# Performance work log

Hardware: AMD Instinct MI355X
Metric: run time of the kernel (lower is better)

Reference implementation:

```python
import jax, jax.numpy as jnp
import numpy as np

N = 50000      # nodes
E = 800000     # edges
MUL = 32       # multiplicity of each irrep (32x0e + 32x1o)
SQRT3 = 3.0 ** 0.5


def setup_inputs() -> dict:
    key = jax.random.key(0)
    k = jax.random.split(key, 7)
    node_features = jax.random.normal(k[0], (N, 4 * MUL), dtype=jnp.float32)  # [N, 32 + 32*3]
    positions = jax.random.normal(k[1], (N, 3), dtype=jnp.float32)
    edge_src = jax.random.randint(k[2], (E,), 0, N, dtype=jnp.int32)
    edge_dst = jax.random.randint(k[3], (E,), 0, N, dtype=jnp.int32)
    tp_weight = jax.random.normal(k[4], (4 * MUL,), dtype=jnp.float32)  # tp.weight_numel = 128
    W_s = jax.random.normal(k[5], (2 * MUL, MUL), dtype=jnp.float32)    # linear: mid 0e (2 blocks) -> out 0e
    W_v = jax.random.normal(k[6], (2 * MUL, MUL), dtype=jnp.float32)    # linear: mid 1o (2 blocks) -> out 1o
    return dict(node_features=node_features, positions=positions,
                edge_src=edge_src, edge_dst=edge_dst,
                tp_weight=tp_weight, W_s=W_s, W_v=W_v)


def reference(node_features, positions, edge_src, edge_dst, tp_weight, W_s, W_v):
    # --- edge vectors and spherical harmonics (normalize=True, 'component') ---
    edge_vec = positions[edge_dst] - positions[edge_src]                       # [E,3]
    unit = edge_vec * jax.lax.rsqrt(jnp.sum(edge_vec * edge_vec, -1, keepdims=True) + 1e-12)
    sh1 = SQRT3 * unit                                                         # l=1 SH, component norm; sh0 == 1
    # --- gather source node features, split irreps ---
    src = node_features[edge_src]                                              # [E,128]
    s = src[:, :MUL]                                                           # [E,32]  scalars 32x0e
    v = src[:, MUL:].reshape(-1, MUL, 3)                                       # [E,32,3] vectors 32x1o
    w0, w1, w2, w3 = jnp.split(tp_weight, 4)                                   # per-path 'uvu' weights (u=32, v=1)
    # --- CG tensor product paths ---
    mid0 = w0 * s                                                              # 0e x 0e -> 0e
    mid1 = (w1 * s)[:, :, None] * sh1[:, None, :]                              # 0e x 1o -> 1o
    mid2 = w2[None, :, None] * v                                               # 1o x 0e -> 1o
    mid3 = w3 * (jnp.einsum('eum,em->eu', v, sh1) / SQRT3)                     # 1o x 1o -> 0e (w3j = delta/sqrt(3))
    messages = jnp.concatenate(
        [mid0, mid1.reshape(-1, 3 * MUL), mid2.reshape(-1, 3 * MUL), mid3], axis=-1)  # [E,256]
    # --- scatter-add messages to destination nodes ---
    agg = jax.ops.segment_sum(messages, edge_dst, num_segments=N)              # [N,256]
    a0 = agg[:, :MUL]
    a1 = agg[:, MUL:4 * MUL].reshape(N, MUL, 3)
    a2 = agg[:, 4 * MUL:7 * MUL].reshape(N, MUL, 3)
    a3 = agg[:, 7 * MUL:]
    # --- equivariant linear mix mid -> out (fan-in normalized per irrep) ---
    inv = np.float32(1.0 / np.sqrt(2 * MUL))
    out_s = (jnp.concatenate([a0, a3], axis=-1) @ W_s) * inv                   # [N,32]
    out_v = jnp.einsum('num,uo->nom', jnp.concatenate([a1, a2], axis=1), W_v) * inv  # [N,32,3]
    return jnp.concatenate([out_s, out_v.reshape(N, 3 * MUL)], axis=-1)        # [N,128]
```

## Files before the change

kernel.cpp:

```cpp
#include <hip/hip_runtime.h>
#include <hip/hip_fp16.h>

#define SQRT3 1.7320508075688772f
#define INV_SQRT3 0.5773502691896258f
#define CAP 64

#define WAVE_SYNC() do { asm volatile("s_waitcnt lgkmcnt(0)" ::: "memory"); \
                         __builtin_amdgcn_wave_barrier(); } while (0)

__global__ void prep_kernel(const float* __restrict__ feat, const float* __restrict__ pos,
                            const float* __restrict__ Ws, const float* __restrict__ Wv,
                            const float* __restrict__ tpw,
                            uint2* __restrict__ featH, float4* __restrict__ pos4,
                            int* __restrict__ cnt,
                            float* __restrict__ WS, float* __restrict__ WV, int N) {
    int i = blockIdx.x * blockDim.x + threadIdx.x;
    int totalF = N * 32;
    if (i < totalF) {
        int node = i >> 5, cl = i & 31;
        const float* fb = feat + (size_t)node * 128;
        float s  = fb[cl];
        float v0 = fb[32 + 3 * cl], v1 = fb[33 + 3 * cl], v2 = fb[34 + 3 * cl];
        __half2 h0 = __floats2half2_rn(s, v0);
        __half2 h1 = __floats2half2_rn(v1, v2);
        uint2 r;
        r.x = *(const unsigned int*)&h0;
        r.y = *(const unsigned int*)&h1;
        featH[i] = r;
        return;
    }
    int j = i - totalF;
    if (j < N) {
        pos4[j] = make_float4(pos[3 * j], pos[3 * j + 1], pos[3 * j + 2], 0.f);
        cnt[j] = 0;
        return;
    }
    int k = j - N;
    if (k < 2048) {
        int u = k >> 5;
        float ws = Ws[k], wv = Wv[k];
        if (u < 32) {
            WS[k] = 0.125f * tpw[u] * ws;
            WV[k] = 0.125f * tpw[32 + u] * wv;
        } else {
            int uu = u - 32;
            WS[k] = 0.125f * tpw[96 + uu] * INV_SQRT3 * ws;
            WV[k] = 0.125f * tpw[64 + uu] * wv;
        }
    }
}


__global__ void scatter_kernel(const int* __restrict__ esrc, const int* __restrict__ edst,
                               int* __restrict__ cnt, int* __restrict__ csrP, int E) {
    int t = blockIdx.x * blockDim.x + threadIdx.x;
    int e0 = t * 4;
    if (e0 + 4 <= E) {
        int4 s4 = *(const int4*)(esrc + e0);
        int4 d4 = *(const int4*)(edst + e0);
        int p;
        p = atomicAdd(&cnt[d4.x], 1); if (p < CAP) csrP[(size_t)d4.x * CAP + p] = s4.x;
        p = atomicAdd(&cnt[d4.y], 1); if (p < CAP) csrP[(size_t)d4.y * CAP + p] = s4.y;
        p = atomicAdd(&cnt[d4.z], 1); if (p < CAP) csrP[(size_t)d4.z * CAP + p] = s4.z;
        p = atomicAdd(&cnt[d4.w], 1); if (p < CAP) csrP[(size_t)d4.w * CAP + p] = s4.w;
    } else {
        for (int e = e0; e < E; ++e) {
            int d = edst[e];
            int p = atomicAdd(&cnt[d], 1);
            if (p < CAP) csrP[(size_t)d * CAP + p] = esrc[e];
        }
    }
}


__global__ __launch_bounds__(256) void node_kernel(
    const uint2* __restrict__ featH, const float4* __restrict__ pos4,
    const int* __restrict__ csrP, const int* __restrict__ cnt,
    const float* __restrict__ WS, const float* __restrict__ WV,
    float* __restrict__ out, int N)
{
    __shared__ float4 geom[4][64];
    __shared__ float  sS[4][68], sX[4][68], sY[4][68], sZ[4][68];
    int lane = threadIdx.x & 63;
    int w    = threadIdx.x >> 6;
    int node = blockIdx.x * 4 + w;
    if (node >= N) return;

    int deg = cnt[node];
    int len = deg < CAP ? deg : CAP;
    int half = lane >> 5;
    int cl   = lane & 31;

    float4 pd = pos4[node];

    if (lane < len) {
        int s = csrP[(size_t)node * CAP + lane];
        float4 ps = pos4[s];
        float ex = pd.x - ps.x, ey = pd.y - ps.y, ez = pd.z - ps.z;
        float rr = SQRT3 * rsqrtf(ex * ex + ey * ey + ez * ez + 1e-12f);
        geom[w][lane] = make_float4(rr * ex, rr * ey, rr * ez, __int_as_float(s));
    }
    WAVE_SYNC();

    float A0 = 0.f, A1x = 0.f, A1y = 0.f, A1z = 0.f;
    float V0 = 0.f, V1 = 0.f, V2 = 0.f, T3 = 0.f;

    int even = len & ~1;
    #pragma unroll 4
    for (int m = 0; m < even; m += 2) {
        float4 g = geom[w][m + half];
        int si = __float_as_int(g.w);
        uint2 fr = featH[(size_t)si * 32 + cl];
        float2 lo = __half22float2(*(const __half2*)&fr.x);
        float2 hi = __half22float2(*(const __half2*)&fr.y);
        A0 += lo.x;
        A1x = fmaf(lo.x, g.x, A1x); A1y = fmaf(lo.x, g.y, A1y); A1z = fmaf(lo.x, g.z, A1z);
        V0 += lo.y; V1 += hi.x; V2 += hi.y;
        T3 = fmaf(lo.y, g.x, fmaf(hi.x, g.y, fmaf(hi.y, g.z, T3)));
    }
    if (len & 1) {
        if (half == 0) {
            float4 g = geom[w][len - 1];
            int si = __float_as_int(g.w);
            uint2 fr = featH[(size_t)si * 32 + cl];
            float2 lo = __half22float2(*(const __half2*)&fr.x);
            float2 hi = __half22float2(*(const __half2*)&fr.y);
            A0 += lo.x;
            A1x = fmaf(lo.x, g.x, A1x); A1y = fmaf(lo.x, g.y, A1y); A1z = fmaf(lo.x, g.z, A1z);
            V0 += lo.y; V1 += hi.x; V2 += hi.y;
            T3 = fmaf(lo.y, g.x, fmaf(hi.x, g.y, fmaf(hi.y, g.z, T3)));
        }
    }

    A0 += __shfl_xor(A0, 32);  A1x += __shfl_xor(A1x, 32);
    A1y += __shfl_xor(A1y, 32); A1z += __shfl_xor(A1z, 32);
    V0 += __shfl_xor(V0, 32);  V1 += __shfl_xor(V1, 32);
    V2 += __shfl_xor(V2, 32);  T3 += __shfl_xor(T3, 32);

    int k = half ? (32 + cl) : cl;
    sS[w][k] = half ? T3 : A0;
    sX[w][k] = half ? V0 : A1x;
    sY[w][k] = half ? V1 : A1y;
    sZ[w][k] = half ? V2 : A1z;
    WAVE_SYNC();

    size_t ob = (size_t)node * 128;
    #pragma unroll
    for (int t = 0; t < 2; ++t) {
        int j = lane + 64 * t;
        const float *ap, *wp;
        if (j < 32) {
            ap = sS[w]; wp = WS + j;
        } else {
            int v = j - 32;
            int o = v / 3, mm = v - 3 * o;
            ap = (mm == 0) ? sX[w] : (mm == 1) ? sY[w] : sZ[w];
            wp = WV + o;
        }
        float r = 0.f;
        #pragma unroll
        for (int q = 0; q < 16; ++q) {
            float4 a = *(const float4*)(ap + 4 * q);
            r = fmaf(a.x, wp[(4 * q + 0) * 32], r);
            r = fmaf(a.y, wp[(4 * q + 1) * 32], r);
            r = fmaf(a.z, wp[(4 * q + 2) * 32], r);
            r = fmaf(a.w, wp[(4 * q + 3) * 32], r);
        }
        out[ob + j] = r;
    }
}

extern "C" void kernel_launch(void* const* d_in, const int* in_sizes, int n_in,
                              void* d_out, int out_size, void* d_ws, size_t ws_size,
                              hipStream_t stream) {
    const float* feat = (const float*)d_in[0];
    const float* pos  = (const float*)d_in[1];
    const int*   esrc = (const int*)d_in[2];
    const int*   edst = (const int*)d_in[3];
    const float* tpw  = (const float*)d_in[4];
    const float* Ws   = (const float*)d_in[5];
    const float* Wv   = (const float*)d_in[6];
    float* out = (float*)d_out;

    int N = in_sizes[0] / 128;
    int E = in_sizes[2];

    uint2*  featH = (uint2*)d_ws;
    float4* pos4  = (float4*)(featH + (size_t)N * 32);
    int*    csrP  = (int*)(pos4 + N);
    int*    cnt   = csrP + (size_t)N * CAP;
    float*  WS    = (float*)(cnt + N);
    float*  WV    = WS + 2048;

    const int tb = 256;
    int prepTot = N * 32 + N + 2048;
    int ebk = (E / 4 + tb) / tb;
    prep_kernel<<<(prepTot + tb - 1) / tb, tb, 0, stream>>>(feat, pos, Ws, Wv, tpw,
                                                            featH, pos4, cnt, WS, WV, N);
    scatter_kernel<<<ebk, tb, 0, stream>>>(esrc, edst, cnt, csrP, E);
    node_kernel<<<(N + 3) / 4, 256, 0, stream>>>(featH, pos4, csrP, cnt, WS, WV, out, N);
}
```

Measured before the change: 124.1 us.

## Fuse scatter and prep kernels, use 16-bit CSR indices and wider feature gathers

Merges the edge-scatter and feature/weight prep into one launch, zeroing counts with a memset instead of inside prep. CSR source indices are stored as 16-bit when N fits, which halves that buffer's traffic. Each lane now gathers a uint4 (two channels), so four edges are processed per step across quarter-waves, followed by a two-level shuffle reduction. The mixing weights are transposed so each output reads contiguous float4s. The extra accumulators raise register pressure, and the int fallback path for large N overlaps csrU storage, so the workspace layout changes.

```diff
diff --git a/kernel.cpp b/kernel.cpp
--- a/kernel.cpp
+++ b/kernel.cpp
@@ -8,13 +8,37 @@
 #define WAVE_SYNC() do { asm volatile("s_waitcnt lgkmcnt(0)" ::: "memory"); \
                          __builtin_amdgcn_wave_barrier(); } while (0)
 
-__global__ void prep_kernel(const float* __restrict__ feat, const float* __restrict__ pos,
-                            const float* __restrict__ Ws, const float* __restrict__ Wv,
-                            const float* __restrict__ tpw,
-                            uint2* __restrict__ featH, float4* __restrict__ pos4,
-                            int* __restrict__ cnt,
-                            float* __restrict__ WS, float* __restrict__ WV, int N) {
-    int i = blockIdx.x * blockDim.x + threadIdx.x;
+template<typename IDX>
+__global__ void build_kernel(const int* __restrict__ esrc, const int* __restrict__ edst,
+                             const float* __restrict__ feat, const float* __restrict__ pos,
+                             const float* __restrict__ Ws, const float* __restrict__ Wv,
+                             const float* __restrict__ tpw,
+                             int* __restrict__ cnt, IDX* __restrict__ csrP,
+                             uint2* __restrict__ featH, float4* __restrict__ pos4,
+                             float* __restrict__ WST, float* __restrict__ WVT,
+                             int N, int E, int sblocks) {
+    int b = blockIdx.x;
+    if (b < sblocks) {
+        int t = b * blockDim.x + threadIdx.x;
+        int e0 = t * 4;
+        if (e0 + 4 <= E) {
+            int4 s4 = *(const int4*)(esrc + e0);
+            int4 d4 = *(const int4*)(edst + e0);
+            int p;
+            p = atomicAdd(&cnt[d4.x], 1); if (p < CAP) csrP[(size_t)d4.x * CAP + p] = (IDX)s4.x;
+            p = atomicAdd(&cnt[d4.y], 1); if (p < CAP) csrP[(size_t)d4.y * CAP + p] = (IDX)s4.y;
+            p = atomicAdd(&cnt[d4.z], 1); if (p < CAP) csrP[(size_t)d4.z * CAP + p] = (IDX)s4.z;
+            p = atomicAdd(&cnt[d4.w], 1); if (p < CAP) csrP[(size_t)d4.w * CAP + p] = (IDX)s4.w;
+        } else {
+            for (int e = e0; e < E; ++e) {
+                int d = edst[e];
+                int p = atomicAdd(&cnt[d], 1);
+                if (p < CAP) csrP[(size_t)d * CAP + p] = (IDX)esrc[e];
+            }
+        }
+        return;
+    }
+    int i = (b - sblocks) * blockDim.x + threadIdx.x;
     int totalF = N * 32;
     if (i < totalF) {
         int node = i >> 5, cl = i & 31;
@@ -32,51 +56,32 @@
     int j = i - totalF;
     if (j < N) {
         pos4[j] = make_float4(pos[3 * j], pos[3 * j + 1], pos[3 * j + 2], 0.f);
-        cnt[j] = 0;
         return;
     }
     int k = j - N;
     if (k < 2048) {
-        int u = k >> 5;
+        int u = k >> 5, c = k & 31;
         float ws = Ws[k], wv = Wv[k];
+        float fs, fv;
         if (u < 32) {
-            WS[k] = 0.125f * tpw[u] * ws;
-            WV[k] = 0.125f * tpw[32 + u] * wv;
+            fs = 0.125f * tpw[u] * ws;
+            fv = 0.125f * tpw[32 + u] * wv;
         } else {
             int uu = u - 32;
-            WS[k] = 0.125f * tpw[96 + uu] * INV_SQRT3 * ws;
-            WV[k] = 0.125f * tpw[64 + uu] * wv;
-        }
+            fs = 0.125f * tpw[96 + uu] * INV_SQRT3 * ws;
+            fv = 0.125f * tpw[64 + uu] * wv;
+        }
+        WST[c * 64 + u] = fs;
+        WVT[c * 64 + u] = fv;
     }
 }
 
 
-__global__ void scatter_kernel(const int* __restrict__ esrc, const int* __restrict__ edst,
-                               int* __restrict__ cnt, int* __restrict__ csrP, int E) {
-    int t = blockIdx.x * blockDim.x + threadIdx.x;
-    int e0 = t * 4;
-    if (e0 + 4 <= E) {
-        int4 s4 = *(const int4*)(esrc + e0);
-        int4 d4 = *(const int4*)(edst + e0);
-        int p;
-        p = atomicAdd(&cnt[d4.x], 1); if (p < CAP) csrP[(size_t)d4.x * CAP + p] = s4.x;
-        p = atomicAdd(&cnt[d4.y], 1); if (p < CAP) csrP[(size_t)d4.y * CAP + p] = s4.y;
-        p = atomicAdd(&cnt[d4.z], 1); if (p < CAP) csrP[(size_t)d4.z * CAP + p] = s4.z;
-        p = atomicAdd(&cnt[d4.w], 1); if (p < CAP) csrP[(size_t)d4.w * CAP + p] = s4.w;
-    } else {
-        for (int e = e0; e < E; ++e) {
-            int d = edst[e];
-            int p = atomicAdd(&cnt[d], 1);
-            if (p < CAP) csrP[(size_t)d * CAP + p] = esrc[e];
-        }
-    }
-}
-
-
+template<typename IDX>
 __global__ __launch_bounds__(256) void node_kernel(
-    const uint2* __restrict__ featH, const float4* __restrict__ pos4,
-    const int* __restrict__ csrP, const int* __restrict__ cnt,
-    const float* __restrict__ WS, const float* __restrict__ WV,
+    const uint4* __restrict__ featH4, const float4* __restrict__ pos4,
+    const IDX* __restrict__ csrP, const int* __restrict__ cnt,
+    const float* __restrict__ WST, const float* __restrict__ WVT,
     float* __restrict__ out, int N)
 {
     __shared__ float4 geom[4][64];
@@ -88,13 +93,13 @@
 
     int deg = cnt[node];
     int len = deg < CAP ? deg : CAP;
-    int half = lane >> 5;
-    int cl   = lane & 31;
+    int qw = lane >> 4;
+    int cq = lane & 15;
 
     float4 pd = pos4[node];
 
     if (lane < len) {
-        int s = csrP[(size_t)node * CAP + lane];
+        int s = (int)csrP[(size_t)node * CAP + lane];
         float4 ps = pos4[s];
         float ex = pd.x - ps.x, ey = pd.y - ps.y, ez = pd.z - ps.z;
         float rr = SQRT3 * rsqrtf(ex * ex + ey * ey + ez * ez + 1e-12f);
@@ -102,46 +107,70 @@
     }
     WAVE_SYNC();
 
-    float A0 = 0.f, A1x = 0.f, A1y = 0.f, A1z = 0.f;
-    float V0 = 0.f, V1 = 0.f, V2 = 0.f, T3 = 0.f;
-
-    int even = len & ~1;
-    #pragma unroll 4
-    for (int m = 0; m < even; m += 2) {
-        float4 g = geom[w][m + half];
+    float A0a = 0.f, A1xa = 0.f, A1ya = 0.f, A1za = 0.f;
+    float V0a = 0.f, V1a = 0.f, V2a = 0.f, T3a = 0.f;
+    float A0b = 0.f, A1xb = 0.f, A1yb = 0.f, A1zb = 0.f;
+    float V0b = 0.f, V1b = 0.f, V2b = 0.f, T3b = 0.f;
+
+    int even4 = len & ~3;
+    #pragma unroll 2
+    for (int m = 0; m < even4; m += 4) {
+        float4 g = geom[w][m + qw];
         int si = __float_as_int(g.w);
-        uint2 fr = featH[(size_t)si * 32 + cl];
-        float2 lo = __half22float2(*(const __half2*)&fr.x);
-        float2 hi = __half22float2(*(const __half2*)&fr.y);
-        A0 += lo.x;
-        A1x = fmaf(lo.x, g.x, A1x); A1y = fmaf(lo.x, g.y, A1y); A1z = fmaf(lo.x, g.z, A1z);
-        V0 += lo.y; V1 += hi.x; V2 += hi.y;
-        T3 = fmaf(lo.y, g.x, fmaf(hi.x, g.y, fmaf(hi.y, g.z, T3)));
-    }
-    if (len & 1) {
-        if (half == 0) {
-            float4 g = geom[w][len - 1];
-            int si = __float_as_int(g.w);
-            uint2 fr = featH[(size_t)si * 32 + cl];
-            float2 lo = __half22float2(*(const __half2*)&fr.x);
-            float2 hi = __half22float2(*(const __half2*)&fr.y);
-            A0 += lo.x;
-            A1x = fmaf(lo.x, g.x, A1x); A1y = fmaf(lo.x, g.y, A1y); A1z = fmaf(lo.x, g.z, A1z);
-            V0 += lo.y; V1 += hi.x; V2 += hi.y;
-            T3 = fmaf(lo.y, g.x, fmaf(hi.x, g.y, fmaf(hi.y, g.z, T3)));
-        }
-    }
-
-    A0 += __shfl_xor(A0, 32);  A1x += __shfl_xor(A1x, 32);
-    A1y += __shfl_xor(A1y, 32); A1z += __shfl_xor(A1z, 32);
-    V0 += __shfl_xor(V0, 32);  V1 += __shfl_xor(V1, 32);
-    V2 += __shfl_xor(V2, 32);  T3 += __shfl_xor(T3, 32);
-
-    int k = half ? (32 + cl) : cl;
-    sS[w][k] = half ? T3 : A0;
-    sX[w][k] = half ? V0 : A1x;
-    sY[w][k] = half ? V1 : A1y;
-    sZ[w][k] = half ? V2 : A1z;
+        uint4 fr = featH4[(size_t)si * 16 + cq];
+        float2 l0 = __half22float2(*(const __half2*)&fr.x);
+        float2 l1 = __half22float2(*(const __half2*)&fr.y);
+        float2 l2 = __half22float2(*(const __half2*)&fr.z);
+        float2 l3 = __half22float2(*(const __half2*)&fr.w);
+        A0a += l0.x;
+        A1xa = fmaf(l0.x, g.x, A1xa); A1ya = fmaf(l0.x, g.y, A1ya); A1za = fmaf(l0.x, g.z, A1za);
+        V0a += l0.y; V1a += l1.x; V2a += l1.y;
+        T3a = fmaf(l0.y, g.x, fmaf(l1.x, g.y, fmaf(l1.y, g.z, T3a)));
+        A0b += l2.x;
+        A1xb = fmaf(l2.x, g.x, A1xb); A1yb = fmaf(l2.x, g.y, A1yb); A1zb = fmaf(l2.x, g.z, A1zb);
+        V0b += l2.y; V1b += l3.x; V2b += l3.y;
+        T3b = fmaf(l2.y, g.x, fmaf(l3.x, g.y, fmaf(l3.y, g.z, T3b)));
+    }
+    int rem = len - even4;
+    if (rem) {
+        bool ok = qw < rem;
+        float4 g = geom[w][even4 + qw];
+        int si = ok ? __float_as_int(g.w) : 0;
+        uint4 fr = featH4[(size_t)si * 16 + cq];
+        if (ok) {
+            float2 l0 = __half22float2(*(const __half2*)&fr.x);
+            float2 l1 = __half22float2(*(const __half2*)&fr.y);
+            float2 l2 = __half22float2(*(const __half2*)&fr.z);
+            float2 l3 = __half22float2(*(const __half2*)&fr.w);
+            A0a += l0.x;
+            A1xa = fmaf(l0.x, g.x, A1xa); A1ya = fmaf(l0.x, g.y, A1ya); A1za = fmaf(l0.x, g.z, A1za);
+            V0a += l0.y; V1a += l1.x; V2a += l1.y;
+            T3a = fmaf(l0.y, g.x, fmaf(l1.x, g.y, fmaf(l1.y, g.z, T3a)));
+            A0b += l2.x;
+            A1xb = fmaf(l2.x, g.x, A1xb); A1yb = fmaf(l2.x, g.y, A1yb); A1zb = fmaf(l2.x, g.z, A1zb);
+            V0b += l2.y; V1b += l3.x; V2b += l3.y;
+            T3b = fmaf(l2.y, g.x, fmaf(l3.x, g.y, fmaf(l3.y, g.z, T3b)));
+        }
+    }
+
+#define RED2(v) do { v += __shfl_xor(v, 16); v += __shfl_xor(v, 32); } while (0)
+    RED2(A0a); RED2(A1xa); RED2(A1ya); RED2(A1za);
+    RED2(V0a); RED2(V1a);  RED2(V2a);  RED2(T3a);
+    RED2(A0b); RED2(A1xb); RED2(A1yb); RED2(A1zb);
+    RED2(V0b); RED2(V1b);  RED2(V2b);  RED2(T3b);
+#undef RED2
+
+    if (qw == 0) {
+        *(float2*)&sS[w][2 * cq] = make_float2(A0a, A0b);
+        *(float2*)&sX[w][2 * cq] = make_float2(A1xa, A1xb);
+        *(float2*)&sY[w][2 * cq] = make_float2(A1ya, A1yb);
+        *(float2*)&sZ[w][2 * cq] = make_float2(A1za, A1zb);
+    } else if (qw == 1) {
+        *(float2*)&sS[w][32 + 2 * cq] = make_float2(T3a, T3b);
+        *(float2*)&sX[w][32 + 2 * cq] = make_float2(V0a, V0b);
+        *(float2*)&sY[w][32 + 2 * cq] = make_float2(V1a, V1b);
+        *(float2*)&sZ[w][32 + 2 * cq] = make_float2(V2a, V2b);
+    }
     WAVE_SYNC();
 
     size_t ob = (size_t)node * 128;
@@ -150,21 +179,20 @@
         int j = lane + 64 * t;
         const float *ap, *wp;
         if (j < 32) {
-            ap = sS[w]; wp = WS + j;
+            ap = sS[w]; wp = WST + j * 64;
         } else {
             int v = j - 32;
             int o = v / 3, mm = v - 3 * o;
             ap = (mm == 0) ? sX[w] : (mm == 1) ? sY[w] : sZ[w];
-            wp = WV + o;
+            wp = WVT + o * 64;
         }
         float r = 0.f;
         #pragma unroll
         for (int q = 0; q < 16; ++q) {
             float4 a = *(const float4*)(ap + 4 * q);
-            r = fmaf(a.x, wp[(4 * q + 0) * 32], r);
-            r = fmaf(a.y, wp[(4 * q + 1) * 32], r);
-            r = fmaf(a.z, wp[(4 * q + 2) * 32], r);
-            r = fmaf(a.w, wp[(4 * q + 3) * 32], r);
+            float4 b = *(const float4*)(wp + 4 * q);
+            r = fmaf(a.x, b.x, r); r = fmaf(a.y, b.y, r);
+            r = fmaf(a.z, b.z, r); r = fmaf(a.w, b.w, r);
         }
         out[ob + j] = r;
     }
@@ -187,16 +215,29 @@
 
     uint2*  featH = (uint2*)d_ws;
     float4* pos4  = (float4*)(featH + (size_t)N * 32);
-    int*    csrP  = (int*)(pos4 + N);
-    int*    cnt   = csrP + (size_t)N * CAP;
-    float*  WS    = (float*)(cnt + N);
-    float*  WV    = WS + 2048;
+    unsigned short* csrU = (unsigned short*)(pos4 + N);
+    int*    cnt   = (int*)(csrU + (size_t)N * CAP);
+    float*  WST   = (float*)(cnt + N);
+    float*  WVT   = WST + 2048;
+
+    hipMemsetAsync(cnt, 0, (size_t)N * sizeof(int), stream);
 
     const int tb = 256;
+    int sblocks = (E / 4 + tb - 1) / tb;
     int prepTot = N * 32 + N + 2048;
-    int ebk = (E / 4 + tb) / tb;
-    prep_kernel<<<(prepTot + tb - 1) / tb, tb, 0, stream>>>(feat, pos, Ws, Wv, tpw,
-                                                            featH, pos4, cnt, WS, WV, N);
-    scatter_kernel<<<ebk, tb, 0, stream>>>(esrc, edst, cnt, csrP, E);
-    node_kernel<<<(N + 3) / 4, 256, 0, stream>>>(featH, pos4, csrP, cnt, WS, WV, out, N);
+    int pblocks = (prepTot + tb - 1) / tb;
+    int nblocks = (N + 3) / 4;
+
+    if (N <= 65535) {
+        build_kernel<unsigned short><<<sblocks + pblocks, tb, 0, stream>>>(
+            esrc, edst, feat, pos, Ws, Wv, tpw, cnt, csrU, featH, pos4, WST, WVT, N, E, sblocks);
+        node_kernel<unsigned short><<<nblocks, 256, 0, stream>>>(
+            (const uint4*)featH, pos4, csrU, cnt, WST, WVT, out, N);
+    } else {
+        int* csrI = (int*)csrU;
+        build_kernel<int><<<sblocks + pblocks, tb, 0, stream>>>(
+            esrc, edst, feat, pos, Ws, Wv, tpw, cnt, csrI, featH, pos4, WST, WVT, N, E, sblocks);
+        node_kernel<int><<<nblocks, 256, 0, stream>>>(
+            (const uint4*)featH, pos4, csrI, cnt, WST, WVT, out, N);
+    }
 }
```

Measured after the change: 200.8 us. 61.8% more time.
